# Kernel tuning notes

Measured on AMD Instinct MI355X. Metric: run time of the kernel, lower is better.

The kernel has to match this reference:

```python
import jax, jax.numpy as jnp
import numpy as np

COMMITMENT_COST = 0.25


def setup_inputs() -> dict:
    key = jax.random.key(0)
    k1, k2 = jax.random.split(key)
    inputs = jax.random.normal(k1, (16, 1024, 256), dtype=jnp.float32)
    embeddings = jax.random.normal(k2, (8192, 256), dtype=jnp.float32) * 0.1
    return {"inputs": inputs, "embeddings": embeddings}


def reference(inputs, embeddings):
    K, D = embeddings.shape
    input_shape = inputs.shape
    flat = inputs.reshape(-1, D)  # [N, D]
    distances = (
        jnp.sum(flat * flat, axis=1, keepdims=True)
        + jnp.sum(embeddings * embeddings, axis=1)
        - 2.0 * jnp.matmul(flat, embeddings.T)
    )
    encoding_indices = jnp.argmin(distances, axis=1)  # [N]
    # direct codebook gather (same math as one-hot @ embeddings)
    quantized = embeddings[encoding_indices].reshape(input_shape)
    quantized_sg = inputs + jax.lax.stop_gradient(quantized - inputs)
    e_latent_loss = jnp.mean((jax.lax.stop_gradient(quantized) - inputs) ** 2)
    q_latent_loss = jnp.mean((quantized_sg - jax.lax.stop_gradient(quantized)) ** 2)
    loss = q_latent_loss + COMMITMENT_COST * e_latent_loss
    # avg one-hot probabilities = normalized codeword counts
    N = flat.shape[0]
    counts = jnp.zeros((K,), dtype=flat.dtype).at[encoding_indices].add(1.0)
    avg_probs = counts / N
    perplexity = jnp.exp(-jnp.sum(avg_probs * jnp.log(avg_probs + 1e-10)))
    return quantized_sg, encoding_indices, loss, perplexity
```

## Files before the change

### kernel.cpp

```cpp
#include <hip/hip_runtime.h>
#include <math.h>
#include <stdint.h>

#define ND_ROWS 16384
#define DDIM    256
#define KCODES  8192
#define NSEG    128
#define NRG     8

typedef _Float16 f16x4 __attribute__((ext_vector_type(4)));
typedef _Float16 f16x8 __attribute__((ext_vector_type(8)));
typedef float    f32x4v __attribute__((ext_vector_type(4)));
typedef float    f32x16 __attribute__((ext_vector_type(16)));


__device__ __attribute__((always_inline)) inline void load_lds16(const void* g, void* l) {
    __builtin_amdgcn_global_load_lds((const __attribute__((address_space(1))) void*)g,
                                     (__attribute__((address_space(3))) void*)l, 16, 0, 0);
}

__global__ __launch_bounds__(256) void prep_kernel(const float* __restrict__ x,
                                                   const float* __restrict__ emb,
                                                   _Float16* __restrict__ Xp,
                                                   _Float16* __restrict__ Bp,
                                                   float* __restrict__ neF) {
    int wave = (blockIdx.x << 2) + (threadIdx.x >> 6);
    int lane = threadIdx.x & 63;
    if (wave < ND_ROWS) {
        const float* src = x + (size_t)wave * DDIM;
        float4 v = ((const float4*)src)[lane];
        f16x4 hi, lo;
        hi[0] = (_Float16)v.x; lo[0] = (_Float16)(v.x - (float)hi[0]);
        hi[1] = (_Float16)v.y; lo[1] = (_Float16)(v.y - (float)hi[1]);
        hi[2] = (_Float16)v.z; lo[2] = (_Float16)(v.z - (float)hi[2]);
        hi[3] = (_Float16)v.w; lo[3] = (_Float16)(v.w - (float)hi[3]);
        int rb = wave >> 5, rl = wave & 31;
        size_t off = (size_t)rb * 16384 + ((lane >> 2) << 9)
                   + (((lane >> 1) & 1) << 8) + (rl << 3) + ((lane & 1) << 2);
        *(f16x4*)(Xp + off)        = hi;
        *(f16x4*)(Xp + off + 8192) = lo;
    } else {
        int r = wave - ND_ROWS;
        const float* src = emb + (size_t)r * DDIM;
        float4 v = ((const float4*)src)[lane];
        float s = v.x*v.x + v.y*v.y + v.z*v.z + v.w*v.w;
        #pragma unroll
        for (int m = 32; m; m >>= 1) s += __shfl_xor(s, m, 64);
        float4 t;
        t.x = -2.0f * v.x; t.y = -2.0f * v.y; t.z = -2.0f * v.z; t.w = -2.0f * v.w;
        f16x4 hi, lo;
        hi[0] = (_Float16)t.x; lo[0] = (_Float16)(t.x - (float)hi[0]);
        hi[1] = (_Float16)t.y; lo[1] = (_Float16)(t.y - (float)hi[1]);
        hi[2] = (_Float16)t.z; lo[2] = (_Float16)(t.z - (float)hi[2]);
        hi[3] = (_Float16)t.w; lo[3] = (_Float16)(t.w - (float)hi[3]);
        _Float16* dst = Bp + (size_t)r * 512;
        *(f16x4*)(dst + lane * 4)       = hi;
        *(f16x4*)(dst + 256 + lane * 4) = lo;
        if (lane == 0) neF[r] = s;
    }
}

#define MFMA16(A, B, C) __builtin_amdgcn_mfma_f32_32x32x16_f16(A, B, C, 0, 0, 0)

#define DECL_STAGE(P) f16x8 P##xh0, P##xl0, P##xh1, P##xl1, \
                            P##c0, P##d0, P##c1, P##d1;

#define LOADX(P, qq) { \
    P##xh0 = *(const f16x8*)(xb0 + (qq) * 1024); \
    P##xl0 = *(const f16x8*)(xb0 + 16384 + (qq) * 1024); \
    P##xh1 = *(const f16x8*)(xb1 + (qq) * 1024); \
    P##xl1 = *(const f16x8*)(xb1 + 16384 + (qq) * 1024); }

#define LOADC(P, qq) { \
    P##c0 = *(const f16x8*)(cpb + (qq) * 1024); \
    P##d0 = *(const f16x8*)(cpb + 16384 + (qq) * 1024); \
    P##c1 = *(const f16x8*)(cpb + 32768 + (qq) * 1024); \
    P##d1 = *(const f16x8*)(cpb + 49152 + (qq) * 1024); }

#define MFMAS(P) \
    __builtin_amdgcn_s_setprio(1); \
    acc[0][0] = MFMA16(P##c0, P##xh0, acc[0][0]); \
    acc[0][1] = MFMA16(P##c1, P##xh0, acc[0][1]); \
    acc[1][0] = MFMA16(P##c0, P##xh1, acc[1][0]); \
    acc[1][1] = MFMA16(P##c1, P##xh1, acc[1][1]); \
    acc[0][0] = MFMA16(P##c0, P##xl0, acc[0][0]); \
    acc[0][1] = MFMA16(P##c1, P##xl0, acc[0][1]); \
    acc[1][0] = MFMA16(P##c0, P##xl1, acc[1][0]); \
    acc[1][1] = MFMA16(P##c1, P##xl1, acc[1][1]); \
    acc[0][0] = MFMA16(P##d0, P##xh0, acc[0][0]); \
    acc[0][1] = MFMA16(P##d1, P##xh0, acc[0][1]); \
    acc[1][0] = MFMA16(P##d0, P##xh1, acc[1][0]); \
    acc[1][1] = MFMA16(P##d1, P##xh1, acc[1][1]); \
    __builtin_amdgcn_s_setprio(0);

__global__ __launch_bounds__(512, 2) void argmin_seg(
    const _Float16* __restrict__ Xp, const _Float16* __restrict__ Bp,
    const float* __restrict__ neF, unsigned long long* __restrict__ minpair) {
    __shared__ __align__(16) _Float16 Cs[64 * 512];

    const int tid  = threadIdx.x;
    const int lane = tid & 63;
    const int w    = tid >> 6;
    const int c32  = lane & 31;
    const int kg   = lane >> 5;

    const int rg      = blockIdx.x & 7;
    const int seg     = blockIdx.x >> 3;
    const int rowBase = rg * 2048;
    const int code0   = seg * 64;

    #pragma unroll
    for (int i = 0; i < 8; ++i) {
        int j    = w * 8 + i;
        int code = code0 + (j & 32) + (lane & 31);
        int s    = ((j & 31) << 1) | (lane >> 5);
        load_lds16((const char*)Bp + ((size_t)code << 10) + (s << 4),
                   (char*)Cs + (j << 10));
    }
    __syncthreads();

    const char* cpb = (const char*)Cs + (kg << 9) + (c32 << 4);

    const int wBase = rowBase + w * 256;
    #pragma unroll 1
    for (int c2 = 0; c2 < 4; ++c2) {
        const int rb0 = (wBase >> 5) + c2 * 2;
        const char* xb0 = (const char*)Xp + (size_t)rb0 * 32768 + lane * 16;
        const char* xb1 = xb0 + 32768;
        f32x16 acc[2][2];
        #pragma unroll
        for (int i = 0; i < 16; ++i) {
            acc[0][0][i] = 0.0f; acc[0][1][i] = 0.0f;
            acc[1][0][i] = 0.0f; acc[1][1][i] = 0.0f;
        }

        DECL_STAGE(a)
        DECL_STAGE(b)
        LOADX(a, 0)
        LOADC(a, 0)
        #pragma unroll 1
        for (int q = 0; q < 16; q += 2) {
            LOADX(b, q + 1)
            LOADC(b, q + 1)
            MFMAS(a)
            LOADX(a, (q + 2) & 15)
            LOADC(a, (q + 2) & 15)
            MFMAS(b)
        }

        f32x4v ne4[2][4];
        #pragma unroll
        for (int mt = 0; mt < 2; ++mt)
            #pragma unroll
            for (int g2 = 0; g2 < 4; ++g2)
                ne4[mt][g2] = *(const f32x4v*)(neF + code0 + mt * 32 + g2 * 8 + 4 * kg);
        #pragma unroll
        for (int ck = 0; ck < 2; ++ck) {
            float best = 3.402823466e+38f;
            int   bi   = 0;
            #pragma unroll
            for (int mt = 0; mt < 2; ++mt)
                #pragma unroll
                for (int r = 0; r < 16; ++r) {
                    float d  = acc[ck][mt][r] + ne4[mt][r >> 2][r & 3];
                    int   id = code0 + mt * 32 + 4 * kg + ((r & 3) + 8 * (r >> 2));
                    if (d < best) { best = d; bi = id; }
                }
            float ov = __shfl_xor(best, 32, 64);
            int   oi = __shfl_xor(bi, 32, 64);
            if (ov < best || (ov == best && oi < bi)) { best = ov; bi = oi; }
            if (kg == 0) {
                int row = (rb0 + ck) * 32 + c32;
                unsigned u = __float_as_uint(best);
                u = (u & 0x80000000u) ? ~u : (u | 0x80000000u);
                atomicMin(&minpair[row],
                          (((unsigned long long)u) << 32) | (unsigned)bi);
            }
        }
    }
}

__global__ __launch_bounds__(256) void finalize_kernel(
    const float* __restrict__ x, const float* __restrict__ emb,
    const unsigned long long* __restrict__ minpair,
    float* __restrict__ out_q, float* __restrict__ out_idx,
    int* __restrict__ counts, float* __restrict__ parts) {
    __shared__ float rde[4], rdq[4];
    int wv   = threadIdx.x >> 6;
    int row  = (blockIdx.x << 2) + wv;
    int lane = threadIdx.x & 63;

    int bi = (int)(minpair[row] & 0xFFFFFFFFull);

    float4 xv = ((const float4*)(x   + (size_t)row * DDIM))[lane];
    float4 ev = ((const float4*)(emb + (size_t)bi  * DDIM))[lane];
    float4 q;
    q.x = xv.x + (ev.x - xv.x);
    q.y = xv.y + (ev.y - xv.y);
    q.z = xv.z + (ev.z - xv.z);
    q.w = xv.w + (ev.w - xv.w);
    ((float4*)(out_q + (size_t)row * DDIM))[lane] = q;

    float de = (ev.x - xv.x) * (ev.x - xv.x) + (ev.y - xv.y) * (ev.y - xv.y)
             + (ev.z - xv.z) * (ev.z - xv.z) + (ev.w - xv.w) * (ev.w - xv.w);
    float dq = (q.x - ev.x) * (q.x - ev.x) + (q.y - ev.y) * (q.y - ev.y)
             + (q.z - ev.z) * (q.z - ev.z) + (q.w - ev.w) * (q.w - ev.w);
    #pragma unroll
    for (int m = 32; m; m >>= 1) {
        de += __shfl_xor(de, m, 64);
        dq += __shfl_xor(dq, m, 64);
    }
    if (lane == 0) {
        out_idx[row] = (float)bi;
        atomicAdd(&counts[bi], 1);
        rde[wv] = de; rdq[wv] = dq;
    }
    __syncthreads();
    if (threadIdx.x == 0) {
        parts[blockIdx.x]        = rde[0] + rde[1] + rde[2] + rde[3];
        parts[4096 + blockIdx.x] = rdq[0] + rdq[1] + rdq[2] + rdq[3];
    }
}

__global__ __launch_bounds__(256) void scalars_kernel(
    const int* __restrict__ counts, const float* __restrict__ parts,
    float* __restrict__ out_loss, float* __restrict__ out_perp) {
    __shared__ float red[256], rde[256], rdq[256];
    float local = 0.0f, de = 0.0f, dq = 0.0f;
    for (int k = threadIdx.x; k < KCODES; k += 256) {
        float p = (float)counts[k] * (1.0f / (float)ND_ROWS);
        local += p * logf(p + 1e-10f);
    }
    for (int k = threadIdx.x; k < 4096; k += 256) {
        de += parts[k];
        dq += parts[4096 + k];
    }
    red[threadIdx.x] = local; rde[threadIdx.x] = de; rdq[threadIdx.x] = dq;
    __syncthreads();
    for (int s = 128; s; s >>= 1) {
        if (threadIdx.x < s) {
            red[threadIdx.x] += red[threadIdx.x + s];
            rde[threadIdx.x] += rde[threadIdx.x + s];
            rdq[threadIdx.x] += rdq[threadIdx.x + s];
        }
        __syncthreads();
    }
    if (threadIdx.x == 0) {
        *out_perp = expf(-red[0]);
        float invn = 1.0f / (float)(ND_ROWS * DDIM);
        *out_loss = rdq[0] * invn + 0.25f * (rde[0] * invn);
    }
}

extern "C" void kernel_launch(void* const* d_in, const int* in_sizes, int n_in,
                              void* d_out, int out_size, void* d_ws, size_t ws_size,
                              hipStream_t stream) {
    const float* x   = (const float*)d_in[0];
    const float* emb = (const float*)d_in[1];

    char* ws = (char*)d_ws;
    unsigned long long* minpair = (unsigned long long*)ws;
    int*      counts = (int*)(ws + 131072);
    float*    parts  = (float*)(ws + 163840);
    float*    neF    = (float*)(ws + 196608);
    _Float16* Xp     = (_Float16*)(ws + 229376);
    _Float16* Bp     = (_Float16*)(ws + 17006592);

    float* out_q    = (float*)d_out;
    float* out_idx  = out_q + (size_t)ND_ROWS * DDIM;
    float* out_loss = out_idx + ND_ROWS;
    float* out_perp = out_loss + 1;

    hipMemsetAsync(minpair, 0xFF, ND_ROWS * sizeof(unsigned long long), stream);
    hipMemsetAsync(counts, 0, KCODES * sizeof(int), stream);

    prep_kernel<<<(KCODES + ND_ROWS) / 4, 256, 0, stream>>>(x, emb, Xp, Bp, neF);
    argmin_seg<<<NRG * NSEG, 512, 0, stream>>>(Xp, Bp, neF, minpair);
    finalize_kernel<<<ND_ROWS / 4, 256, 0, stream>>>(x, emb, minpair,
                                                     out_q, out_idx, counts, parts);
    scalars_kernel<<<1, 256, 0, stream>>>(counts, parts, out_loss, out_perp);
}
```

Measured before the change: 323.5 us.

## Double the per-block codebook tile to 128 codes to reuse X fragments

Measured after the change: 336.1 us. 3.9% more time.

```diff
diff --git a/kernel.cpp b/kernel.cpp
--- a/kernel.cpp
+++ b/kernel.cpp
@@ -5,7 +5,7 @@
 #define ND_ROWS 16384
 #define DDIM    256
 #define KCODES  8192
-#define NSEG    128
+#define NSEG    64
 #define NRG     8
 
 typedef _Float16 f16x4 __attribute__((ext_vector_type(4)));
@@ -62,8 +62,7 @@
 
 #define MFMA16(A, B, C) __builtin_amdgcn_mfma_f32_32x32x16_f16(A, B, C, 0, 0, 0)
 
-#define DECL_STAGE(P) f16x8 P##xh0, P##xl0, P##xh1, P##xl1, \
-                            P##c0, P##d0, P##c1, P##d1;
+#define DECL_X(P) f16x8 P##xh0, P##xl0, P##xh1, P##xl1;
 
 #define LOADX(P, qq) { \
     P##xh0 = *(const f16x8*)(xb0 + (qq) * 1024); \
@@ -71,32 +70,32 @@
     P##xh1 = *(const f16x8*)(xb1 + (qq) * 1024); \
     P##xl1 = *(const f16x8*)(xb1 + 16384 + (qq) * 1024); }
 
-#define LOADC(P, qq) { \
-    P##c0 = *(const f16x8*)(cpb + (qq) * 1024); \
-    P##d0 = *(const f16x8*)(cpb + 16384 + (qq) * 1024); \
-    P##c1 = *(const f16x8*)(cpb + 32768 + (qq) * 1024); \
-    P##d1 = *(const f16x8*)(cpb + 49152 + (qq) * 1024); }
-
-#define MFMAS(P) \
+#define LOADCP(C0, D0, C1, D1, base, qq) { \
+    C0 = *(const f16x8*)(cpb + (base) + (qq) * 1024); \
+    D0 = *(const f16x8*)(cpb + (base) + 16384 + (qq) * 1024); \
+    C1 = *(const f16x8*)(cpb + (base) + 32768 + (qq) * 1024); \
+    D1 = *(const f16x8*)(cpb + (base) + 49152 + (qq) * 1024); }
+
+#define MFMA12(P, C0, D0, C1, D1, m0, m1) \
     __builtin_amdgcn_s_setprio(1); \
-    acc[0][0] = MFMA16(P##c0, P##xh0, acc[0][0]); \
-    acc[0][1] = MFMA16(P##c1, P##xh0, acc[0][1]); \
-    acc[1][0] = MFMA16(P##c0, P##xh1, acc[1][0]); \
-    acc[1][1] = MFMA16(P##c1, P##xh1, acc[1][1]); \
-    acc[0][0] = MFMA16(P##c0, P##xl0, acc[0][0]); \
-    acc[0][1] = MFMA16(P##c1, P##xl0, acc[0][1]); \
-    acc[1][0] = MFMA16(P##c0, P##xl1, acc[1][0]); \
-    acc[1][1] = MFMA16(P##c1, P##xl1, acc[1][1]); \
-    acc[0][0] = MFMA16(P##d0, P##xh0, acc[0][0]); \
-    acc[0][1] = MFMA16(P##d1, P##xh0, acc[0][1]); \
-    acc[1][0] = MFMA16(P##d0, P##xh1, acc[1][0]); \
-    acc[1][1] = MFMA16(P##d1, P##xh1, acc[1][1]); \
+    acc[0][m0] = MFMA16(C0, P##xh0, acc[0][m0]); \
+    acc[1][m0] = MFMA16(C0, P##xh1, acc[1][m0]); \
+    acc[0][m1] = MFMA16(C1, P##xh0, acc[0][m1]); \
+    acc[1][m1] = MFMA16(C1, P##xh1, acc[1][m1]); \
+    acc[0][m0] = MFMA16(C0, P##xl0, acc[0][m0]); \
+    acc[1][m0] = MFMA16(C0, P##xl1, acc[1][m0]); \
+    acc[0][m1] = MFMA16(C1, P##xl0, acc[0][m1]); \
+    acc[1][m1] = MFMA16(C1, P##xl1, acc[1][m1]); \
+    acc[0][m0] = MFMA16(D0, P##xh0, acc[0][m0]); \
+    acc[1][m0] = MFMA16(D0, P##xh1, acc[1][m0]); \
+    acc[0][m1] = MFMA16(D1, P##xh0, acc[0][m1]); \
+    acc[1][m1] = MFMA16(D1, P##xh1, acc[1][m1]); \
     __builtin_amdgcn_s_setprio(0);
 
 __global__ __launch_bounds__(512, 2) void argmin_seg(
     const _Float16* __restrict__ Xp, const _Float16* __restrict__ Bp,
     const float* __restrict__ neF, unsigned long long* __restrict__ minpair) {
-    __shared__ __align__(16) _Float16 Cs[64 * 512];
+    extern __shared__ __align__(16) _Float16 Cs[];
 
     const int tid  = threadIdx.x;
     const int lane = tid & 63;
@@ -107,13 +106,13 @@
     const int rg      = blockIdx.x & 7;
     const int seg     = blockIdx.x >> 3;
     const int rowBase = rg * 2048;
-    const int code0   = seg * 64;
+    const int code0   = seg * 128;
 
     #pragma unroll
-    for (int i = 0; i < 8; ++i) {
-        int j    = w * 8 + i;
-        int code = code0 + (j & 32) + (lane & 31);
-        int s    = ((j & 31) << 1) | (lane >> 5);
+    for (int i = 0; i < 16; ++i) {
+        int j    = w * 16 + i;
+        int code = code0 + ((j >> 5) << 5) + (lane & 31);
+        int s    = (((j >> 4) & 1) << 5) | ((j & 15) << 1) | (lane >> 5);
         load_lds16((const char*)Bp + ((size_t)code << 10) + (s << 4),
                    (char*)Cs + (j << 10));
     }
@@ -127,30 +126,36 @@
         const int rb0 = (wBase >> 5) + c2 * 2;
         const char* xb0 = (const char*)Xp + (size_t)rb0 * 32768 + lane * 16;
         const char* xb1 = xb0 + 32768;
-        f32x16 acc[2][2];
-        #pragma unroll
-        for (int i = 0; i < 16; ++i) {
-            acc[0][0][i] = 0.0f; acc[0][1][i] = 0.0f;
-            acc[1][0][i] = 0.0f; acc[1][1][i] = 0.0f;
-        }
-
-        DECL_STAGE(a)
-        DECL_STAGE(b)
+
+        f32x16 acc[2][4];
+        #pragma unroll
+        for (int mt = 0; mt < 4; ++mt)
+            #pragma unroll
+            for (int i = 0; i < 16; ++i) { acc[0][mt][i] = 0.0f; acc[1][mt][i] = 0.0f; }
+
+        DECL_X(a)
+        DECL_X(b)
+        f16x8 cA0, dA0, cA1, dA1;
+        f16x8 cB0, dB0, cB1, dB1;
         LOADX(a, 0)
-        LOADC(a, 0)
+        LOADCP(cA0, dA0, cA1, dA1, 0, 0)
         #pragma unroll 1
         for (int q = 0; q < 16; q += 2) {
             LOADX(b, q + 1)
-            LOADC(b, q + 1)
-            MFMAS(a)
+            LOADCP(cB0, dB0, cB1, dB1, 65536, q)
+            MFMA12(a, cA0, dA0, cA1, dA1, 0, 1)
+            LOADCP(cA0, dA0, cA1, dA1, 0, q + 1)
+            MFMA12(a, cB0, dB0, cB1, dB1, 2, 3)
             LOADX(a, (q + 2) & 15)
-            LOADC(a, (q + 2) & 15)
-            MFMAS(b)
+            LOADCP(cB0, dB0, cB1, dB1, 65536, q + 1)
+            MFMA12(b, cA0, dA0, cA1, dA1, 0, 1)
+            LOADCP(cA0, dA0, cA1, dA1, 0, (q + 2) & 15)
+            MFMA12(b, cB0, dB0, cB1, dB1, 2, 3)
         }
 
-        f32x4v ne4[2][4];
-        #pragma unroll
-        for (int mt = 0; mt < 2; ++mt)
+        f32x4v ne4[4][4];
+        #pragma unroll
+        for (int mt = 0; mt < 4; ++mt)
             #pragma unroll
             for (int g2 = 0; g2 < 4; ++g2)
                 ne4[mt][g2] = *(const f32x4v*)(neF + code0 + mt * 32 + g2 * 8 + 4 * kg);
@@ -159,7 +164,7 @@
             float best = 3.402823466e+38f;
             int   bi   = 0;
             #pragma unroll
-            for (int mt = 0; mt < 2; ++mt)
+            for (int mt = 0; mt < 4; ++mt)
                 #pragma unroll
                 for (int r = 0; r < 16; ++r) {
                     float d  = acc[ck][mt][r] + ne4[mt][r >> 2][r & 3];
@@ -275,7 +280,7 @@
     hipMemsetAsync(counts, 0, KCODES * sizeof(int), stream);
 
     prep_kernel<<<(KCODES + ND_ROWS) / 4, 256, 0, stream>>>(x, emb, Xp, Bp, neF);
-    argmin_seg<<<NRG * NSEG, 512, 0, stream>>>(Xp, Bp, neF, minpair);
+    argmin_seg<<<NRG * NSEG, 512, 131072, stream>>>(Xp, Bp, neF, minpair);
     finalize_kernel<<<ND_ROWS / 4, 256, 0, stream>>>(x, emb, minpair,
                                                      out_q, out_idx, counts, parts);
     scalars_kernel<<<1, 256, 0, stream>>>(counts, parts, out_loss, out_perp);
```
